# Performance work log

Hardware: AMD Instinct MI355X
Metric: run time of the kernel (lower is better)

## Reference

```python
import jax, jax.numpy as jnp
import numpy as np

# static configuration (matches init_kwargs)
Z, H, W = 8, 96, 192
WZ, WH, WW = 2, 6, 12
DIM, HEADS, DEPTH = 192, 6, 2
HD = DIM // HEADS
NZ, NH, NW = Z // WZ, H // WH, W // WW
N = WZ * WH * WW            # tokens per window = 144
WT = NZ * NH                 # window_types = 64
SHIFT = (WZ // 2, WH // 2, WW // 2)
SCALE = HD ** -0.5


def _pos_index():
    czi = np.arange(WZ); czj = -np.arange(WZ) * WZ
    chi = np.arange(WH); chj = -np.arange(WH) * WH
    cw = np.arange(WW)
    c1 = np.stack(np.meshgrid(czi, chi, cw, indexing='ij'), 0).reshape(3, -1)
    c2 = np.stack(np.meshgrid(czj, chj, cw, indexing='ij'), 0).reshape(3, -1)
    coords = (c1[:, :, None] - c2[:, None, :]).transpose(1, 2, 0).astype(np.int64)
    coords[:, :, 2] += WW - 1
    coords[:, :, 1] *= 2 * WW - 1
    coords[:, :, 0] *= (2 * WW - 1) * WH * WH
    return coords.sum(-1).reshape(-1).astype(np.int32)


def _shift_mask():
    img = np.zeros((Z, H, W))
    zs = (slice(0, -WZ), slice(-WZ, -SHIFT[0]), slice(-SHIFT[0], None))
    hs = (slice(0, -WH), slice(-WH, -SHIFT[1]), slice(-SHIFT[1], None))
    ws = (slice(0, -WW), slice(-WW, -SHIFT[2]), slice(-SHIFT[2], None))
    cnt = 0
    for a in zs:
        for b in hs:
            for c in ws:
                img[a, b, c] = cnt; cnt += 1
    mw = img.reshape(NZ, WZ, NH, WH, NW, WW).transpose(0, 2, 4, 1, 3, 5).reshape(-1, N)
    am = mw[:, None, :] - mw[:, :, None]
    return np.where(am != 0, -100.0, 0.0).astype(np.float32)  # (WT*NW, N, N)

POS_IDX = jnp.asarray(_pos_index())
MASK = jnp.asarray(_shift_mask())


def _partition(x):
    # (B,Z,H,W,C) -> (B*num_windows, N, C), windows ordered (nZ,nH,nW)
    B, C = x.shape[0], x.shape[-1]
    x = x.reshape(B, NZ, WZ, NH, WH, NW, WW, C).transpose(0, 1, 3, 5, 2, 4, 6, 7)
    return x.reshape(-1, N, C)


def _reverse(w, B):
    C = w.shape[-1]
    x = w.reshape(B, NZ, NH, NW, WZ, WH, WW, C).transpose(0, 1, 4, 2, 5, 3, 6, 7)
    return x.reshape(B, Z, H, W, C)


def _ln(x, s, b):
    m = x.mean(-1, keepdims=True)
    v = ((x - m) ** 2).mean(-1, keepdims=True)
    return (x - m) * jax.lax.rsqrt(v + 1e-5) * s + b


def _attention(xw, qw, qb, bias_tab, pw, pb, masked):
    B_ = xw.shape[0]
    qkv = (xw @ qw + qb).reshape(B_, N, 3, HEADS, HD).transpose(2, 0, 3, 1, 4)
    q, k, v = qkv[0] * SCALE, qkv[1], qkv[2]              # (B_, H, N, hd)
    s = jnp.einsum('bhnd,bhmd->bhnm', q, k)               # (B_, H, N, N)
    # earth-specific relative position bias, gathered per window type
    bias = bias_tab[POS_IDX].reshape(N, N, WT, HEADS).transpose(2, 3, 0, 1)  # (WT,H,N,N)
    B = B_ // (WT * NW)
    s = s.reshape(B, WT, NW, HEADS, N, N) + bias[None, :, None]
    if masked:
        s = s + MASK.reshape(WT, NW, N, N)[None, :, :, None]
    a = jax.nn.softmax(s.reshape(B_, HEADS, N, N), axis=-1)
    o = jnp.einsum('bhnm,bhmd->bnhd', a, v).reshape(B_, N, DIM)
    return o @ pw + pb


def _block(x, p, roll):
    n1w, n1b, qw, qb, bt, pw, pb, n2w, n2b, w1, b1, w2, b2 = p
    B = x.shape[0]
    h = _ln(x, n1w, n1b).reshape(B, Z, H, W, DIM)
    if roll:
        h = jnp.roll(h, (-SHIFT[0], -SHIFT[1], -SHIFT[2]), axis=(1, 2, 3))
    h = _attention(_partition(h), qw, qb, bt, pw, pb, roll)
    h = _reverse(h, B)
    if roll:
        h = jnp.roll(h, SHIFT, axis=(1, 2, 3))
    x = x + h.reshape(B, Z * H * W, DIM)
    h2 = _ln(x, n2w, n2b)
    h2 = jax.nn.gelu(h2 @ w1 + b1, approximate=False) @ w2 + b2
    return x + h2


def setup_inputs() -> dict:
    key = jax.random.key(0)
    ks = jax.random.split(key, 8)
    d = {
        'x': jax.random.normal(ks[0], (1, Z * H * W, DIM), jnp.float32),
        'norm1_w': jnp.ones((DEPTH, DIM), jnp.float32),
        'norm1_b': jnp.zeros((DEPTH, DIM), jnp.float32),
        'qkv_w': jax.random.normal(ks[1], (DEPTH, DIM, 3 * DIM), jnp.float32) * 0.02,
        'qkv_b': jnp.zeros((DEPTH, 3 * DIM), jnp.float32),
        'bias_tab': jax.random.normal(ks[2], (DEPTH, WZ**2 * WH**2 * (2 * WW - 1), WT, HEADS), jnp.float32) * 0.02,
        'proj_w': jax.random.normal(ks[3], (DEPTH, DIM, DIM), jnp.float32) * 0.02,
        'proj_b': jnp.zeros((DEPTH, DIM), jnp.float32),
        'norm2_w': jnp.ones((DEPTH, DIM), jnp.float32),
        'norm2_b': jnp.zeros((DEPTH, DIM), jnp.float32),
        'mlp_w1': jax.random.normal(ks[4], (DEPTH, DIM, 4 * DIM), jnp.float32) * 0.02,
        'mlp_b1': jnp.zeros((DEPTH, 4 * DIM), jnp.float32),
        'mlp_w2': jax.random.normal(ks[5], (DEPTH, 4 * DIM, DIM), jnp.float32) * 0.02,
        'mlp_b2': jnp.zeros((DEPTH, DIM), jnp.float32),
    }
    return d


def reference(x, norm1_w, norm1_b, qkv_w, qkv_b, bias_tab, proj_w, proj_b,
              norm2_w, norm2_b, mlp_w1, mlp_b1, mlp_w2, mlp_b2):
    for i in range(DEPTH):
        p = (norm1_w[i], norm1_b[i], qkv_w[i], qkv_b[i], bias_tab[i], proj_w[i],
             proj_b[i], norm2_w[i], norm2_b[i], mlp_w1[i], mlp_b1[i], mlp_w2[i], mlp_b2[i])
        x = _block(x, p, roll=(i % 2 == 1))
    return x
```

## Files before the change

kernel.cpp:

```cpp
#include <hip/hip_runtime.h>
#include <hip/hip_bf16.h>

typedef short short8 __attribute__((ext_vector_type(8)));
typedef short s4b __attribute__((ext_vector_type(4)));
typedef float floatx4 __attribute__((ext_vector_type(4)));
typedef unsigned int u32;

#define DEVFN static __device__ __forceinline__

constexpr int L_TOK = 147456;
constexpr float ATT_SCALE = 0.17677669529663687f;

DEVFN int win_to_spatial(int t, int sz, int sh, int sw) {
  int w_ = t / 144;
  int n  = t - w_ * 144;
  int nz = w_ >> 8, nh = (w_ >> 4) & 15, nw = w_ & 15;
  int iz = n / 72; int rem = n - iz * 72;
  int ih = rem / 12; int iw = rem - ih * 12;
  int z = nz * 2 + iz + sz;  if (z >= 8)   z -= 8;
  int h = nh * 6 + ih + sh;  if (h >= 96)  h -= 96;
  int wc = nw * 12 + iw + sw; if (wc >= 192) wc -= 192;
  return (z * 96 + h) * 192 + wc;
}

DEVFN void gload16(const void* g, void* l) {
  __builtin_amdgcn_global_load_lds(
      (const __attribute__((address_space(1))) u32*)(g),
      (__attribute__((address_space(3))) u32*)(l), 16, 0, 0);
}

DEVFN void bar_vm14() { asm volatile("s_waitcnt vmcnt(14)\n\ts_barrier" ::: "memory"); }
DEVFN void bar_vm12() { asm volatile("s_waitcnt vmcnt(12)\n\ts_barrier" ::: "memory"); }
DEVFN void bar_vm11() { asm volatile("s_waitcnt vmcnt(11)\n\ts_barrier" ::: "memory"); }
DEVFN void bar_vm10() { asm volatile("s_waitcnt vmcnt(10)\n\ts_barrier" ::: "memory"); }
DEVFN void bar_vm8()  { asm volatile("s_waitcnt vmcnt(8)\n\ts_barrier"  ::: "memory"); }
DEVFN void bar_vm7()  { asm volatile("s_waitcnt vmcnt(7)\n\ts_barrier"  ::: "memory"); }
DEVFN void bar_vm6()  { asm volatile("s_waitcnt vmcnt(6)\n\ts_barrier"  ::: "memory"); }
DEVFN void bar_vm0()  { asm volatile("s_waitcnt vmcnt(0)\n\ts_barrier"  ::: "memory"); }
DEVFN void bar_lg()   { asm volatile("s_waitcnt lgkmcnt(0)\n\ts_barrier" ::: "memory"); }

DEVFN float gelu_fast(float x) {
  float e = __expf(-1.702f * x);
  return x * __fdividef(1.0f, 1.0f + e);
}

__global__ __launch_bounds__(256) void convT4_kernel(
    const float* __restrict__ in0, const float* __restrict__ in1,
    const float* __restrict__ in2, const float* __restrict__ in3,
    __hip_bfloat16* __restrict__ o0, __hip_bfloat16* __restrict__ o1,
    __hip_bfloat16* __restrict__ o2, __hip_bfloat16* __restrict__ o3)
{
  int idx = blockIdx.x * 256 + threadIdx.x;
  const float* in; __hip_bfloat16* out; int K, N;
  if (idx < 110592)      { in = in0; out = o0; K = 192; N = 576; }
  else if (idx < 147456) { in = in1; out = o1; K = 192; N = 192; idx -= 110592; }
  else if (idx < 294912) { in = in2; out = o2; K = 192; N = 768; idx -= 147456; }
  else                   { in = in3; out = o3; K = 768; N = 192; idx -= 294912; }
  int n = idx / K, k = idx - n * K;
  out[idx] = __float2bfloat16(in[(long)k * N + n]);
}

__global__ __launch_bounds__(256) void biaspre_kernel(
    const float* __restrict__ tab, __hip_bfloat16* __restrict__ out)
{
  int t = blockIdx.x;
  int e0 = blockIdx.y * 2304;
  for (int e = e0 + threadIdx.x; e < e0 + 2304; e += 256) {
    int m = e / 144, n = e - m * 144;
    int izn = n / 72, rn = n - izn * 72, ihn = rn / 12, iwn = rn - ihn * 12;
    int izm = m / 72, rm = m - izm * 72, ihm = rm / 12, iwm = rm - ihm * 12;
    int idx = (izn + 2 * izm) * 828 + (ihn + 6 * ihm) * 23 + (iwn - iwm + 11);
    out[(long)t * 20736 + e] = __float2bfloat16(tab[(long)idx * 384 + t]);
  }
}

__global__ __launch_bounds__(512) void qkv_kernel(
    const float* __restrict__ x, const float* __restrict__ nw,
    const float* __restrict__ nb,
    const __hip_bfloat16* __restrict__ wqkvT, const float* __restrict__ qbias,
    __hip_bfloat16* __restrict__ oq, __hip_bfloat16* __restrict__ okk,
    __hip_bfloat16* __restrict__ ov, int sz, int sh, int sw)
{
  __shared__ char a_lds[128 * 384];
  __shared__ char w_lds[64 * 384];
  __shared__ float bias_lds[576];

  int tid = threadIdx.x, lane = tid & 63, wv = tid >> 6;
  int lc = lane & 15, lr = lane >> 4, lr4 = lr * 4;
  long row0 = (long)blockIdx.x * 128;
  const char* Wc = (const char*)wqkvT;

#pragma unroll
  for (int i = 0; i < 3; i++) {
    int ii = i * 8 + wv;
    int p = ii * 1024 + lane * 16;
    int row = p / 384, cb = p - row * 384;
    int sc = (cb >> 4) ^ (row & 7);
    gload16(Wc + (long)row * 384 + sc * 16, w_lds + ii * 1024);
  }
  if (tid < 144) *(float4*)(bias_lds + tid * 4) = *(const float4*)(qbias + tid * 4);

#pragma unroll
  for (int rg = 0; rg < 2; rg++) {
    int row = rg * 64 + (tid >> 3), sub = tid & 7;
    int src = win_to_spatial((int)(row0 + row), sz, sh, sw);
    const float* xp = x + (long)src * 192;
    float4 v[6];
#pragma unroll
    for (int p = 0; p < 3; p++) {
      v[2*p]   = *(const float4*)(xp + p * 64 + sub * 8);
      v[2*p+1] = *(const float4*)(xp + p * 64 + sub * 8 + 4);
    }
    float s = 0.f, sq = 0.f;
#pragma unroll
    for (int i = 0; i < 6; i++) {
      s  += v[i].x + v[i].y + v[i].z + v[i].w;
      sq += v[i].x*v[i].x + v[i].y*v[i].y + v[i].z*v[i].z + v[i].w*v[i].w;
    }
    for (int m = 1; m < 8; m <<= 1) { s += __shfl_xor(s, m); sq += __shfl_xor(sq, m); }
    float mean = s * (1.0f/192.0f);
    float var  = sq * (1.0f/192.0f) - mean * mean;
    float rstd = rsqrtf(var + 1e-5f);
#pragma unroll
    for (int p = 0; p < 3; p++) {
      int ch0 = p * 64 + sub * 8;
      float4 wa = *(const float4*)(nw + ch0), wb_ = *(const float4*)(nw + ch0 + 4);
      float4 ba = *(const float4*)(nb + ch0), bb_ = *(const float4*)(nb + ch0 + 4);
      const float* va = (const float*)&v[2*p];
      const float* wa_p = (const float*)&wa; const float* wb_p = (const float*)&wb_;
      const float* ba_p = (const float*)&ba; const float* bb_p = (const float*)&bb_;
      __hip_bfloat16 tmp[8];
#pragma unroll
      for (int j = 0; j < 4; j++) {
        tmp[j]     = __float2bfloat16((va[j]   - mean) * rstd * wa_p[j] + ba_p[j]);
        tmp[j + 4] = __float2bfloat16((va[j+4] - mean) * rstd * wb_p[j] + bb_p[j]);
      }
      int slot = p * 8 + sub;
      int ss = slot ^ (row & 7);
      *(uint4*)(a_lds + row * 384 + ss * 16) = *(uint4*)tmp;
    }
  }
  __syncthreads();

  int m0 = wv * 16;
  short8 afr[6];
#pragma unroll
  for (int kt = 0; kt < 6; kt++) {
    int ra = m0 + lc;
    afr[kt] = *(const short8*)(a_lds + ra * 384 + ((kt * 4 + lr) ^ (ra & 7)) * 16);
  }
  bar_lg();

#pragma unroll
  for (int i = 0; i < 3; i++) {
    int ii = i * 8 + wv;
    int p = ii * 1024 + lane * 16;
    int row = p / 384, cb = p - row * 384;
    int sc = (cb >> 4) ^ (row & 7);
    gload16(Wc + (long)(64 + row) * 384 + sc * 16, a_lds + ii * 1024);
  }

  for (int pn = 0; pn < 9; pn++) {
    char* wcur = (pn & 1) ? a_lds : w_lds;
    if (pn == 1) bar_vm7(); else if (pn == 8) bar_vm8(); else bar_vm11();
    floatx4 acc[4];
#pragma unroll
    for (int cf = 0; cf < 4; cf++) acc[cf] = {0.f, 0.f, 0.f, 0.f};
#pragma unroll
    for (int kt = 0; kt < 6; kt++)
#pragma unroll
      for (int cf = 0; cf < 4; cf++) {
        int rb = cf * 16 + lc;
        short8 wfr = *(const short8*)(wcur + rb * 384 + ((kt * 4 + lr) ^ (rb & 7)) * 16);
        acc[cf] = __builtin_amdgcn_mfma_f32_16x16x32_bf16(wfr, afr[kt], acc[cf], 0, 0, 0);
      }
    bar_lg();
    if (pn < 7) {
#pragma unroll
      for (int i = 0; i < 3; i++) {
        int ii = i * 8 + wv;
        int p = ii * 1024 + lane * 16;
        int row = p / 384, cb = p - row * 384;
        int sc = (cb >> 4) ^ (row & 7);
        gload16(Wc + (long)((pn + 2) * 64 + row) * 384 + sc * 16, wcur + ii * 1024);
      }
    }
    int sec = pn / 3;
    __hip_bfloat16* dst = (sec == 0) ? oq : ((sec == 1) ? okk : ov);
    float scale = (sec == 0) ? ATT_SCALE : 1.0f;
#pragma unroll
    for (int cf = 0; cf < 4; cf++) {
      int colb = pn * 64 + cf * 16 + lr4;
      float4 bb = *(const float4*)(bias_lds + colb);
      int c0 = colb - sec * 192;
      int head = c0 >> 5, ch = c0 & 31;
      long row = row0 + m0 + lc;
      __hip_bfloat16 tmp[4];
      tmp[0] = __float2bfloat16((acc[cf][0] + bb.x) * scale);
      tmp[1] = __float2bfloat16((acc[cf][1] + bb.y) * scale);
      tmp[2] = __float2bfloat16((acc[cf][2] + bb.z) * scale);
      tmp[3] = __float2bfloat16((acc[cf][3] + bb.w) * scale);
      *(s4b*)(dst + ((long)head * L_TOK + row) * 32 + ch) = *(s4b*)tmp;
    }
  }
}

__global__ __launch_bounds__(256) void proj_kernel(
    const __hip_bfloat16* __restrict__ A, const __hip_bfloat16* __restrict__ BT,
    const float* __restrict__ cbias, const float* __restrict__ xin,
    float* __restrict__ xout, int sz, int sh, int sw)
{
  __shared__ __hip_bfloat16 a_lds[128 * 192];
  __shared__ __hip_bfloat16 b_lds[64 * 192];
  int tid = threadIdx.x, lane = tid & 63, wv = tid >> 6;
  int wm = wv >> 1, wn = wv & 1;
  int lc = lane & 15, lr = lane >> 4, lr4 = lr * 4;
  long rowBase = (long)blockIdx.x * 128;
  int colBase = blockIdx.y * 64;
  floatx4 acc[4][2];
#pragma unroll
  for (int i = 0; i < 4; i++)
#pragma unroll
    for (int j = 0; j < 2; j++) acc[i][j] = {0.f, 0.f, 0.f, 0.f};

  const char* Ac = (const char*)A;
  const char* Bc = (const char*)BT;

#pragma unroll
  for (int i = 0; i < 12; i++) {
    int ii = i * 4 + wv;
    int p = ii * 1024 + lane * 16;
    int row = p / 384, cb = p - row * 384;
    int sc = (cb >> 4) ^ (row & 7);
    int ch = sc * 8; int head = ch >> 5;
    const char* g = Ac + (((long)head * L_TOK + rowBase + row) * 32 + (ch & 31)) * 2;
    gload16(g, (char*)a_lds + ii * 1024);
  }
#pragma unroll
  for (int i = 0; i < 6; i++) {
    int ii = i * 4 + wv;
    int p = ii * 1024 + lane * 16;
    int row = p / 384, cb = p - row * 384;
    int sc = (cb >> 4) ^ (row & 7);
    const char* g = Bc + (colBase + row) * (long)192 * 2 + sc * 16;
    gload16(g, (char*)b_lds + ii * 1024);
  }
  __syncthreads();
#pragma unroll
  for (int kt = 0; kt < 6; kt++) {
    short8 bfr[2];
#pragma unroll
    for (int fn = 0; fn < 2; fn++) {
      int rb = wn * 32 + fn * 16 + lc;
      bfr[fn] = *(const short8*)((const char*)b_lds + rb * 384 + ((kt * 4 + lr) ^ (rb & 7)) * 16);
    }
#pragma unroll
    for (int fm = 0; fm < 4; fm++) {
      int ra = wm * 64 + fm * 16 + lc;
      short8 afr = *(const short8*)((const char*)a_lds + ra * 384 + ((kt * 4 + lr) ^ (ra & 7)) * 16);
#pragma unroll
      for (int fn = 0; fn < 2; fn++)
        acc[fm][fn] = __builtin_amdgcn_mfma_f32_16x16x32_bf16(bfr[fn], afr, acc[fm][fn], 0, 0, 0);
    }
  }

#pragma unroll
  for (int fm = 0; fm < 4; fm++) {
    long row = rowBase + wm * 64 + fm * 16 + lc;
    int dsti = win_to_spatial((int)row, sz, sh, sw);
#pragma unroll
    for (int fn = 0; fn < 2; fn++) {
      int colb = colBase + wn * 32 + fn * 16 + lr4;
      float4 cb4 = *(const float4*)(cbias + colb);
      long di = (long)dsti * 192 + colb;
      float4 xv = *(const float4*)(xin + di);
      float4 ov;
      ov.x = acc[fm][fn][0] + cb4.x + xv.x;
      ov.y = acc[fm][fn][1] + cb4.y + xv.y;
      ov.z = acc[fm][fn][2] + cb4.z + xv.z;
      ov.w = acc[fm][fn][3] + cb4.w + xv.w;
      *(float4*)(xout + di) = ov;
    }
  }
}

__global__ __launch_bounds__(256) void mlp1_kernel(
    const float* __restrict__ x, const float* __restrict__ nw,
    const float* __restrict__ nb,
    const __hip_bfloat16* __restrict__ w1T, const float* __restrict__ b1,
    __hip_bfloat16* __restrict__ T)
{
  __shared__ char a_lds[64 * 384];
  __shared__ char w_lds[64 * 384];
  __shared__ float b1_lds[768];

  int tid = threadIdx.x, lane = tid & 63, wv = tid >> 6;
  int lc = lane & 15, lr = lane >> 4, lr4 = lr * 4;
  long row0 = (long)blockIdx.x * 64;
  const char* Wc = (const char*)w1T;

#pragma unroll
  for (int i = 0; i < 6; i++) {
    int ii = i * 4 + wv;
    int p = ii * 1024 + lane * 16;
    int row = p / 384, cb = p - row * 384;
    int sc = (cb >> 4) ^ (row & 7);
    gload16(Wc + (long)row * 384 + sc * 16, w_lds + ii * 1024);
  }
  if (tid < 192) *(float4*)(b1_lds + tid * 4) = *(const float4*)(b1 + tid * 4);

#pragma unroll
  for (int rg = 0; rg < 2; rg++) {
    int row = rg * 32 + (tid >> 3), sub = tid & 7;
    const float* xp = x + (row0 + row) * 192;
    float4 v[6];
#pragma unroll
    for (int p = 0; p < 3; p++) {
      v[2*p]   = *(const float4*)(xp + p * 64 + sub * 8);
      v[2*p+1] = *(const float4*)(xp + p * 64 + sub * 8 + 4);
    }
    float s = 0.f, sq = 0.f;
#pragma unroll
    for (int i = 0; i < 6; i++) {
      s  += v[i].x + v[i].y + v[i].z + v[i].w;
      sq += v[i].x*v[i].x + v[i].y*v[i].y + v[i].z*v[i].z + v[i].w*v[i].w;
    }
    for (int m = 1; m < 8; m <<= 1) { s += __shfl_xor(s, m); sq += __shfl_xor(sq, m); }
    float mean = s * (1.0f/192.0f);
    float var  = sq * (1.0f/192.0f) - mean * mean;
    float rstd = rsqrtf(var + 1e-5f);
#pragma unroll
    for (int p = 0; p < 3; p++) {
      int ch0 = p * 64 + sub * 8;
      float4 wa = *(const float4*)(nw + ch0), wb_ = *(const float4*)(nw + ch0 + 4);
      float4 ba = *(const float4*)(nb + ch0), bb_ = *(const float4*)(nb + ch0 + 4);
      const float* va = (const float*)&v[2*p];
      const float* wa_p = (const float*)&wa; const float* wb_p = (const float*)&wb_;
      const float* ba_p = (const float*)&ba; const float* bb_p = (const float*)&bb_;
      __hip_bfloat16 tmp[8];
#pragma unroll
      for (int j = 0; j < 4; j++) {
        tmp[j]     = __float2bfloat16((va[j]   - mean) * rstd * wa_p[j] + ba_p[j]);
        tmp[j + 4] = __float2bfloat16((va[j+4] - mean) * rstd * wb_p[j] + bb_p[j]);
      }
      int slot = p * 8 + sub;
      int ss = slot ^ (row & 7);
      *(uint4*)(a_lds + row * 384 + ss * 16) = *(uint4*)tmp;
    }
  }
  __syncthreads();

  int m0 = wv * 16;
  short8 afr[6];
#pragma unroll
  for (int kt = 0; kt < 6; kt++) {
    int ra = m0 + lc;
    afr[kt] = *(const short8*)(a_lds + ra * 384 + ((kt * 4 + lr) ^ (ra & 7)) * 16);
  }
  bar_lg();

#pragma unroll
  for (int i = 0; i < 6; i++) {
    int ii = i * 4 + wv;
    int p = ii * 1024 + lane * 16;
    int row = p / 384, cb = p - row * 384;
    int sc = (cb >> 4) ^ (row & 7);
    gload16(Wc + (long)(64 + row) * 384 + sc * 16, a_lds + ii * 1024);
  }

  for (int pn = 0; pn < 12; pn++) {
    char* wcur = (pn & 1) ? a_lds : w_lds;
    if (pn == 0) bar_vm6();
    else if (pn == 1) bar_vm10();
    else if (pn == 11) bar_vm8();
    else bar_vm14();
    floatx4 acc[4];
#pragma unroll
    for (int cf = 0; cf < 4; cf++) acc[cf] = {0.f, 0.f, 0.f, 0.f};
#pragma unroll
    for (int kt = 0; kt < 6; kt++)
#pragma unroll
      for (int cf = 0; cf < 4; cf++) {
        int rb = cf * 16 + lc;
        short8 wfr = *(const short8*)(wcur + rb * 384 + ((kt * 4 + lr) ^ (rb & 7)) * 16);
        acc[cf] = __builtin_amdgcn_mfma_f32_16x16x32_bf16(wfr, afr[kt], acc[cf], 0, 0, 0);
      }
    bar_lg();
    if (pn < 10) {
#pragma unroll
      for (int i = 0; i < 6; i++) {
        int ii = i * 4 + wv;
        int p = ii * 1024 + lane * 16;
        int row = p / 384, cb = p - row * 384;
        int sc = (cb >> 4) ^ (row & 7);
        gload16(Wc + (long)((pn + 2) * 64 + row) * 384 + sc * 16, wcur + ii * 1024);
      }
    }
#pragma unroll
    for (int cf = 0; cf < 4; cf++) {
      int colb = pn * 64 + cf * 16 + lr4;
      float4 bb = *(const float4*)(b1_lds + colb);
      long row = row0 + m0 + lc;
      __hip_bfloat16 tmp[4];
      tmp[0] = __float2bfloat16(gelu_fast(acc[cf][0] + bb.x));
      tmp[1] = __float2bfloat16(gelu_fast(acc[cf][1] + bb.y));
      tmp[2] = __float2bfloat16(gelu_fast(acc[cf][2] + bb.z));
      tmp[3] = __float2bfloat16(gelu_fast(acc[cf][3] + bb.w));
      *(s4b*)(T + row * 768 + colb) = *(s4b*)tmp;
    }
  }
}

__global__ __launch_bounds__(256) void mlp2_kernel(
    const __hip_bfloat16* __restrict__ T, const __hip_bfloat16* __restrict__ w2T,
    const float* __restrict__ b2, const float* __restrict__ x,
    float* __restrict__ out)
{
  __shared__ char a_lds[64 * 384];
  __shared__ char w_lds0[64 * 384];
  __shared__ char w_lds1[64 * 384];

  int tid = threadIdx.x, lane = tid & 63, wv = tid >> 6;
  int lc = lane & 15, lr = lane >> 4, lr4 = lr * 4;
  long row0 = (long)blockIdx.x * 64;
  const char* Ac = (const char*)T;
  const char* Wc = (const char*)w2T;
  int m0 = wv * 16;

  floatx4 acc[3][4];
#pragma unroll
  for (int np = 0; np < 3; np++)
#pragma unroll
    for (int cf = 0; cf < 4; cf++) acc[np][cf] = {0.f, 0.f, 0.f, 0.f};

  int s_ii = lane * 16;
#define STAGE_A(KP)                                                          \
  {                                                                          \
    _Pragma("unroll")                                                        \
    for (int i = 0; i < 6; i++) {                                            \
      int ii = i * 4 + wv;                                                   \
      int p = ii * 1024 + s_ii;                                              \
      int row = p / 384, cb = p - row * 384;                                 \
      int sc = (cb >> 4) ^ (row & 7);                                        \
      gload16(Ac + (row0 + row) * 1536 + (KP) * 384 + sc * 16,               \
              a_lds + ii * 1024);                                            \
    }                                                                        \
  }
#define STAGE_W(KP, NP, BUF)                                                 \
  {                                                                          \
    _Pragma("unroll")                                                        \
    for (int i = 0; i < 6; i++) {                                            \
      int ii = i * 4 + wv;                                                   \
      int p = ii * 1024 + s_ii;                                              \
      int row = p / 384, cb = p - row * 384;                                 \
      int sc = (cb >> 4) ^ (row & 7);                                        \
      gload16(Wc + (long)((NP) * 64 + row) * 1536 + (KP) * 384 + sc * 16,    \
              (BUF) + ii * 1024);                                            \
    }                                                                        \
  }

  STAGE_A(0);
  STAGE_W(0, 0, w_lds0);
  __syncthreads();
  STAGE_W(0, 1, w_lds1);

#pragma unroll
  for (int kp = 0; kp < 4; kp++) {
    if (kp) bar_vm12();
    short8 afr[6];
#pragma unroll
    for (int kt = 0; kt < 6; kt++) {
      int ra = m0 + lc;
      afr[kt] = *(const short8*)(a_lds + ra * 384 + ((kt * 4 + lr) ^ (ra & 7)) * 16);
    }
    bar_lg();
    if (kp < 3) STAGE_A(kp + 1);

#pragma unroll
    for (int np = 0; np < 3; np++) {
      int g = 3 * kp + np;
      const char* wcur = (g & 1) ? w_lds1 : w_lds0;
      if (g == 11) bar_vm0();
      else if (np == 2 || kp == 3) bar_vm6();
      else bar_vm12();
#pragma unroll
      for (int kt = 0; kt < 6; kt++)
#pragma unroll
        for (int cf = 0; cf < 4; cf++) {
          int rb = cf * 16 + lc;
          short8 wfr = *(const short8*)(wcur + rb * 384 + ((kt * 4 + lr) ^ (rb & 7)) * 16);
          acc[np][cf] = __builtin_amdgcn_mfma_f32_16x16x32_bf16(wfr, afr[kt], acc[np][cf], 0, 0, 0);
        }
      bar_lg();
      int gn = g + 2;
      if (gn < 12) {
        char* bnx = (gn & 1) ? w_lds1 : w_lds0;
        int kpn = gn / 3, npn = gn - kpn * 3;
        STAGE_W(kpn, npn, bnx);
      }
    }
  }

#pragma unroll
  for (int np = 0; np < 3; np++)
#pragma unroll
    for (int cf = 0; cf < 4; cf++) {
      int colb = np * 64 + cf * 16 + lr4;
      long row = row0 + m0 + lc;
      float4 bb = *(const float4*)(b2 + colb);
      float4 xv = *(const float4*)(x + row * 192 + colb);
      float4 ov;
      ov.x = acc[np][cf][0] + bb.x + xv.x;
      ov.y = acc[np][cf][1] + bb.y + xv.y;
      ov.z = acc[np][cf][2] + bb.z + xv.z;
      ov.w = acc[np][cf][3] + bb.w + xv.w;
      *(float4*)(out + row * 192 + colb) = ov;
    }
#undef STAGE_A
#undef STAGE_W
}

__global__ __launch_bounds__(576) void attn_kernel(
    const __hip_bfloat16* __restrict__ q, const __hip_bfloat16* __restrict__ k,
    const __hip_bfloat16* __restrict__ v, const __hip_bfloat16* __restrict__ bias_bf,
    __hip_bfloat16* __restrict__ o, int masked)
{
  __shared__ __hip_bfloat16 vT[2][32 * 168];
  __shared__ __hip_bfloat16 pS[9][16 * 40];

  int bid = blockIdx.x;
  int chunk = bid % 384, half = bid / 384;
  int wt = chunk / 6, head = chunk - wt * 6;

  int tid = threadIdx.x, wv = tid >> 6, lane = tid & 63;
  int lr = lane >> 4, lc = lane & 15, lr4 = lr * 4;
  const __hip_bfloat16 zb = __float2bfloat16(0.0f);
  int rt = wv;

  s4b bias_r[9];
  {
    const __hip_bfloat16* bp = bias_bf + (long)chunk * 20736;
#pragma unroll
    for (int c = 0; c < 9; c++)
      bias_r[c] = *(const s4b*)(bp + (c * 16 + lc) * 144 + rt * 16 + lr4);
  }

  int w0 = wt * 16 + half * 8;
  long hb = (long)head * L_TOK * 32;
  {
    long base0 = hb + (long)w0 * 144 * 32;
    int tk = tid >> 2, c = tid & 3;
    uint4 raw = *(const uint4*)(v + base0 + tk * 32 + c * 8);
    __hip_bfloat16 tmp[8]; *(uint4*)tmp = raw;
#pragma unroll
    for (int j = 0; j < 8; j++) vT[0][(c * 8 + j) * 168 + tk] = tmp[j];
  }
  for (int id = tid; id < 1024; id += 576)
    vT[id >> 9][((id >> 4) & 31) * 168 + 144 + (id & 15)] = zb;

  int sign_[4], sigm_[9];
#pragma unroll
  for (int r = 0; r < 4; r++) {
    int p = rt * 16 + lr4 + r;
    int iz = p / 72; int rem = p - iz * 72; int ih = rem / 12; int iw = rem - ih * 12;
    sign_[r] = iz | ((ih >= 3) << 1) | ((iw >= 6) << 2);
  }
#pragma unroll
  for (int c = 0; c < 9; c++) {
    int p = c * 16 + lc;
    int iz = p / 72; int rem = p - iz * 72; int ih = rem / 12; int iw = rem - ih * 12;
    sigm_[c] = iz | ((ih >= 3) << 1) | ((iw >= 6) << 2);
  }
  bar_lg();

  __hip_bfloat16* pw = &pS[wv][0];
  const floatx4 z4 = {0.f, 0.f, 0.f, 0.f};
  int cur = 0;

  for (int wi = 0; wi < 8; wi++) {
    int w_ = w0 + wi;
    long base = hb + (long)w_ * 144 * 32;
    uint4 vreg;
    if (wi < 7)
      vreg = *(const uint4*)(v + base + 144 * 32 + (tid >> 2) * 32 + (tid & 3) * 8);

    int g = 0;
    if (masked) {
      int nz = w_ >> 8, nh = (w_ >> 4) & 15, nw = w_ & 15;
      g = (nz == 3 ? 1 : 0) | (nh == 15 ? 2 : 0) | (nw == 15 ? 4 : 0);
    }

    short8 qf = *(const short8*)(q + base + (rt * 16 + lc) * 32 + lr * 8);
    floatx4 s[9];
    __builtin_amdgcn_s_setprio(1);
#pragma unroll
    for (int c = 0; c < 9; c++) {
      short8 kf = *(const short8*)(k + base + (c * 16 + lc) * 32 + lr * 8);
      s[c] = __builtin_amdgcn_mfma_f32_16x16x32_bf16(qf, kf, z4, 0, 0, 0);
    }
    __builtin_amdgcn_s_setprio(0);

    float rmax[4] = {-1e30f, -1e30f, -1e30f, -1e30f};
#pragma unroll
    for (int c = 0; c < 9; c++) {
      __hip_bfloat16 bb[4];
      *(s4b*)bb = bias_r[c];
#pragma unroll
      for (int r = 0; r < 4; r++) {
        float val = s[c][r] + __bfloat162float(bb[r]);
        if ((sign_[r] ^ sigm_[c]) & g) val -= 100.0f;
        s[c][r] = val;
        rmax[r] = fmaxf(rmax[r], val);
      }
    }
#pragma unroll
    for (int r = 0; r < 4; r++)
      for (int mm = 1; mm < 16; mm <<= 1) rmax[r] = fmaxf(rmax[r], __shfl_xor(rmax[r], mm));
    float rsum[4] = {0.f, 0.f, 0.f, 0.f};
#pragma unroll
    for (int c = 0; c < 9; c++)
#pragma unroll
      for (int r = 0; r < 4; r++) {
        float p = __expf(s[c][r] - rmax[r]);
        s[c][r] = p; rsum[r] += p;
      }
#pragma unroll
    for (int r = 0; r < 4; r++)
      for (int mm = 1; mm < 16; mm <<= 1) rsum[r] += __shfl_xor(rsum[r], mm);

    if (wi < 7) {
      __hip_bfloat16 tmp[8]; *(uint4*)tmp = vreg;
      int tk = tid >> 2, c = tid & 3;
#pragma unroll
      for (int j = 0; j < 8; j++) vT[cur ^ 1][(c * 8 + j) * 168 + tk] = tmp[j];
    }

    floatx4 oacc[2] = {z4, z4};
#pragma unroll
    for (int t = 0; t < 5; t++) {
      if (t < 4) {
#pragma unroll
        for (int h2 = 0; h2 < 2; h2++) {
          int c = 2 * t + h2;
#pragma unroll
          for (int r = 0; r < 4; r++)
            pw[(lr4 + r) * 40 + h2 * 16 + lc] = __float2bfloat16(s[c][r]);
        }
      } else {
#pragma unroll
        for (int r = 0; r < 4; r++) {
          pw[(lr4 + r) * 40 + lc] = __float2bfloat16(s[8][r]);
          pw[(lr4 + r) * 40 + 16 + lc] = zb;
        }
      }
      short8 pa = *(short8*)(&pw[lc * 40 + lr * 8]);
      __builtin_amdgcn_s_setprio(1);
#pragma unroll
      for (int vt = 0; vt < 2; vt++) {
        short8 vbf = *(short8*)(&vT[cur][(vt * 16 + lc) * 168 + t * 32 + lr * 8]);
        oacc[vt] = __builtin_amdgcn_mfma_f32_16x16x32_bf16(pa, vbf, oacc[vt], 0, 0, 0);
      }
      __builtin_amdgcn_s_setprio(0);
    }
    float inv[4];
#pragma unroll
    for (int r = 0; r < 4; r++) inv[r] = 1.0f / rsum[r];
#pragma unroll
    for (int vt = 0; vt < 2; vt++)
#pragma unroll
      for (int r = 0; r < 4; r++)
        o[base + (rt * 16 + lr4 + r) * 32 + vt * 16 + lc] =
            __float2bfloat16(oacc[vt][r] * inv[r]);

    bar_lg();
    cur ^= 1;
  }
}

extern "C" void kernel_launch(void* const* d_in, const int* in_sizes, int n_in,
                              void* d_out, int out_size, void* d_ws, size_t ws_size,
                              hipStream_t stream)
{
  const float* x_in  = (const float*)d_in[0];
  const float* n1w   = (const float*)d_in[1];
  const float* n1b   = (const float*)d_in[2];
  const float* qkvw  = (const float*)d_in[3];
  const float* qkvb  = (const float*)d_in[4];
  const float* btab  = (const float*)d_in[5];
  const float* projw = (const float*)d_in[6];
  const float* projb = (const float*)d_in[7];
  const float* n2w   = (const float*)d_in[8];
  const float* n2b   = (const float*)d_in[9];
  const float* w1    = (const float*)d_in[10];
  const float* b1    = (const float*)d_in[11];
  const float* w2    = (const float*)d_in[12];
  const float* b2    = (const float*)d_in[13];

  char* ws = (char*)d_ws;
  float* x            = (float*)(ws);
  __hip_bfloat16* qb  = (__hip_bfloat16*)(ws + 169869312);
  __hip_bfloat16* kb  = qb + 28311552;
  __hip_bfloat16* vb  = kb + 28311552;
  __hip_bfloat16* ob  = vb + 28311552;
  __hip_bfloat16* Tb  = qb;
  __hip_bfloat16* biasb = (__hip_bfloat16*)(ws + 396361728);
  __hip_bfloat16* wqkvT  = (__hip_bfloat16*)(ws + 428212224);
  __hip_bfloat16* wprojT = wqkvT + 110592;
  __hip_bfloat16* w1T    = wprojT + 36864;
  __hip_bfloat16* w2T    = w1T + 147456;

  for (int layer = 0; layer < 2; layer++) {
    int sz = layer ? 1 : 0, sh = layer ? 3 : 0, sw = layer ? 6 : 0;
    int masked = layer;
    const float* xsrc = (layer == 0) ? x_in : x;

    convT4_kernel<<<1728, 256, 0, stream>>>(
        qkvw + (long)layer * 110592, projw + (long)layer * 36864,
        w1 + (long)layer * 147456, w2 + (long)layer * 147456,
        wqkvT, wprojT, w1T, w2T);
    biaspre_kernel<<<dim3(384, 9), 256, 0, stream>>>(btab + (long)layer * 3312 * 384, biasb);

    qkv_kernel<<<1152, 512, 0, stream>>>(
        xsrc, n1w + layer * 192, n1b + layer * 192, wqkvT, qkvb + layer * 576,
        qb, kb, vb, sz, sh, sw);
    attn_kernel<<<768, 576, 0, stream>>>(qb, kb, vb, biasb, ob, masked);
    proj_kernel<<<dim3(1152, 3), 256, 0, stream>>>(
        ob, wprojT, projb + layer * 192, xsrc, x, sz, sh, sw);
    mlp1_kernel<<<2304, 256, 0, stream>>>(
        x, n2w + layer * 192, n2b + layer * 192, w1T, b1 + layer * 768, Tb);
    mlp2_kernel<<<2304, 256, 0, stream>>>(
        Tb, w2T, b2 + layer * 192, x, (layer == 0) ? x : (float*)d_out);
  }
}
```

Measured before the change: 1.154 ms.

## Process two windows per iteration in attention kernel for more ILP

The attention kernel now handles two windows per loop iteration instead of one, interleaving their QK MFMAs, softmax, and PV MFMAs so independent work can hide latency. V tiles for both windows are staged into the two LDS buffers, replacing the single-window double buffer, and the prefetched V for the next pair is written after a barrier, followed by a second barrier. This halves loop trips and barriers per window but roughly doubles register pressure, which may hurt occupancy. It also loses the previous overlap of V transposition with compute.

```diff
diff --git a/kernel.cpp b/kernel.cpp
--- a/kernel.cpp
+++ b/kernel.cpp
@@ -526,7 +526,7 @@
     __hip_bfloat16* __restrict__ o, int masked)
 {
   __shared__ __hip_bfloat16 vT[2][32 * 168];
-  __shared__ __hip_bfloat16 pS[9][16 * 40];
+  __shared__ __hip_bfloat16 pS[2][9][16 * 40];
 
   int bid = blockIdx.x;
   int chunk = bid % 384, half = bid / 384;
@@ -548,12 +548,15 @@
   int w0 = wt * 16 + half * 8;
   long hb = (long)head * L_TOK * 32;
   {
-    long base0 = hb + (long)w0 * 144 * 32;
     int tk = tid >> 2, c = tid & 3;
-    uint4 raw = *(const uint4*)(v + base0 + tk * 32 + c * 8);
-    __hip_bfloat16 tmp[8]; *(uint4*)tmp = raw;
-#pragma unroll
-    for (int j = 0; j < 8; j++) vT[0][(c * 8 + j) * 168 + tk] = tmp[j];
+#pragma unroll
+    for (int b = 0; b < 2; b++) {
+      long base0 = hb + (long)(w0 + b) * 144 * 32;
+      uint4 raw = *(const uint4*)(v + base0 + tk * 32 + c * 8);
+      __hip_bfloat16 tmp[8]; *(uint4*)tmp = raw;
+#pragma unroll
+      for (int j = 0; j < 8; j++) vT[b][(c * 8 + j) * 168 + tk] = tmp[j];
+    }
   }
   for (int id = tid; id < 1024; id += 576)
     vT[id >> 9][((id >> 4) & 31) * 168 + 144 + (id & 15)] = zb;
@@ -573,69 +576,79 @@
   }
   bar_lg();
 
-  __hip_bfloat16* pw = &pS[wv][0];
+  __hip_bfloat16* pwA = &pS[0][wv][0];
+  __hip_bfloat16* pwB = &pS[1][wv][0];
   const floatx4 z4 = {0.f, 0.f, 0.f, 0.f};
-  int cur = 0;
-
-  for (int wi = 0; wi < 8; wi++) {
-    int w_ = w0 + wi;
-    long base = hb + (long)w_ * 144 * 32;
-    uint4 vreg;
-    if (wi < 7)
-      vreg = *(const uint4*)(v + base + 144 * 32 + (tid >> 2) * 32 + (tid & 3) * 8);
-
-    int g = 0;
+
+  for (int j4 = 0; j4 < 4; j4++) {
+    int wA = w0 + 2 * j4, wB = wA + 1;
+    long baseA = hb + (long)wA * 144 * 32;
+    long baseB = hb + (long)wB * 144 * 32;
+    uint4 vregA, vregB;
+    if (j4 < 3) {
+      vregA = *(const uint4*)(v + baseA + 2 * 144 * 32 + (tid >> 2) * 32 + (tid & 3) * 8);
+      vregB = *(const uint4*)(v + baseB + 2 * 144 * 32 + (tid >> 2) * 32 + (tid & 3) * 8);
+    }
+    int gA = 0, gB = 0;
     if (masked) {
-      int nz = w_ >> 8, nh = (w_ >> 4) & 15, nw = w_ & 15;
-      g = (nz == 3 ? 1 : 0) | (nh == 15 ? 2 : 0) | (nw == 15 ? 4 : 0);
-    }
-
-    short8 qf = *(const short8*)(q + base + (rt * 16 + lc) * 32 + lr * 8);
-    floatx4 s[9];
+      { int nz = wA >> 8, nh = (wA >> 4) & 15, nw = wA & 15;
+        gA = (nz == 3 ? 1 : 0) | (nh == 15 ? 2 : 0) | (nw == 15 ? 4 : 0); }
+      { int nz = wB >> 8, nh = (wB >> 4) & 15, nw = wB & 15;
+        gB = (nz == 3 ? 1 : 0) | (nh == 15 ? 2 : 0) | (nw == 15 ? 4 : 0); }
+    }
+
+    short8 qfA = *(const short8*)(q + baseA + (rt * 16 + lc) * 32 + lr * 8);
+    short8 qfB = *(const short8*)(q + baseB + (rt * 16 + lc) * 32 + lr * 8);
+    floatx4 sA[9], sB[9];
     __builtin_amdgcn_s_setprio(1);
 #pragma unroll
     for (int c = 0; c < 9; c++) {
-      short8 kf = *(const short8*)(k + base + (c * 16 + lc) * 32 + lr * 8);
-      s[c] = __builtin_amdgcn_mfma_f32_16x16x32_bf16(qf, kf, z4, 0, 0, 0);
+      short8 kfA = *(const short8*)(k + baseA + (c * 16 + lc) * 32 + lr * 8);
+      sA[c] = __builtin_amdgcn_mfma_f32_16x16x32_bf16(qfA, kfA, z4, 0, 0, 0);
+      short8 kfB = *(const short8*)(k + baseB + (c * 16 + lc) * 32 + lr * 8);
+      sB[c] = __builtin_amdgcn_mfma_f32_16x16x32_bf16(qfB, kfB, z4, 0, 0, 0);
     }
     __builtin_amdgcn_s_setprio(0);
 
-    float rmax[4] = {-1e30f, -1e30f, -1e30f, -1e30f};
+    float rmaxA[4] = {-1e30f, -1e30f, -1e30f, -1e30f};
+    float rmaxB[4] = {-1e30f, -1e30f, -1e30f, -1e30f};
 #pragma unroll
     for (int c = 0; c < 9; c++) {
       __hip_bfloat16 bb[4];
       *(s4b*)bb = bias_r[c];
 #pragma unroll
       for (int r = 0; r < 4; r++) {
-        float val = s[c][r] + __bfloat162float(bb[r]);
-        if ((sign_[r] ^ sigm_[c]) & g) val -= 100.0f;
-        s[c][r] = val;
-        rmax[r] = fmaxf(rmax[r], val);
+        float bf = __bfloat162float(bb[r]);
+        int msk = (sign_[r] ^ sigm_[c]);
+        float vA = sA[c][r] + bf; if (msk & gA) vA -= 100.0f;
+        float vB = sB[c][r] + bf; if (msk & gB) vB -= 100.0f;
+        sA[c][r] = vA; rmaxA[r] = fmaxf(rmaxA[r], vA);
+        sB[c][r] = vB; rmaxB[r] = fmaxf(rmaxB[r], vB);
       }
     }
 #pragma unroll
     for (int r = 0; r < 4; r++)
-      for (int mm = 1; mm < 16; mm <<= 1) rmax[r] = fmaxf(rmax[r], __shfl_xor(rmax[r], mm));
-    float rsum[4] = {0.f, 0.f, 0.f, 0.f};
+      for (int mm = 1; mm < 16; mm <<= 1) {
+        rmaxA[r] = fmaxf(rmaxA[r], __shfl_xor(rmaxA[r], mm));
+        rmaxB[r] = fmaxf(rmaxB[r], __shfl_xor(rmaxB[r], mm));
+      }
+    float rsumA[4] = {0.f, 0.f, 0.f, 0.f};
+    float rsumB[4] = {0.f, 0.f, 0.f, 0.f};
 #pragma unroll
     for (int c = 0; c < 9; c++)
 #pragma unroll
       for (int r = 0; r < 4; r++) {
-        float p = __expf(s[c][r] - rmax[r]);
-        s[c][r] = p; rsum[r] += p;
+        float pA = __expf(sA[c][r] - rmaxA[r]); sA[c][r] = pA; rsumA[r] += pA;
+        float pB = __expf(sB[c][r] - rmaxB[r]); sB[c][r] = pB; rsumB[r] += pB;
       }
 #pragma unroll
     for (int r = 0; r < 4; r++)
-      for (int mm = 1; mm < 16; mm <<= 1) rsum[r] += __shfl_xor(rsum[r], mm);
-
-    if (wi < 7) {
-      __hip_bfloat16 tmp[8]; *(uint4*)tmp = vreg;
-      int tk = tid >> 2, c = tid & 3;
-#pragma unroll
-      for (int j = 0; j < 8; j++) vT[cur ^ 1][(c * 8 + j) * 168 + tk] = tmp[j];
-    }
-
-    floatx4 oacc[2] = {z4, z4};
+      for (int mm = 1; mm < 16; mm <<= 1) {
+        rsumA[r] += __shfl_xor(rsumA[r], mm);
+        rsumB[r] += __shfl_xor(rsumB[r], mm);
+      }
+
+    floatx4 oaccA[2] = {z4, z4}, oaccB[2] = {z4, z4};
 #pragma unroll
     for (int t = 0; t < 5; t++) {
       if (t < 4) {
@@ -643,37 +656,60 @@
         for (int h2 = 0; h2 < 2; h2++) {
           int c = 2 * t + h2;
 #pragma unroll
-          for (int r = 0; r < 4; r++)
-            pw[(lr4 + r) * 40 + h2 * 16 + lc] = __float2bfloat16(s[c][r]);
+          for (int r = 0; r < 4; r++) {
+            pwA[(lr4 + r) * 40 + h2 * 16 + lc] = __float2bfloat16(sA[c][r]);
+            pwB[(lr4 + r) * 40 + h2 * 16 + lc] = __float2bfloat16(sB[c][r]);
+          }
         }
       } else {
 #pragma unroll
         for (int r = 0; r < 4; r++) {
-          pw[(lr4 + r) * 40 + lc] = __float2bfloat16(s[8][r]);
-          pw[(lr4 + r) * 40 + 16 + lc] = zb;
+          pwA[(lr4 + r) * 40 + lc] = __float2bfloat16(sA[8][r]);
+          pwA[(lr4 + r) * 40 + 16 + lc] = zb;
+          pwB[(lr4 + r) * 40 + lc] = __float2bfloat16(sB[8][r]);
+          pwB[(lr4 + r) * 40 + 16 + lc] = zb;
         }
       }
-      short8 pa = *(short8*)(&pw[lc * 40 + lr * 8]);
+      short8 paA = *(short8*)(&pwA[lc * 40 + lr * 8]);
+      short8 paB = *(short8*)(&pwB[lc * 40 + lr * 8]);
       __builtin_amdgcn_s_setprio(1);
 #pragma unroll
       for (int vt = 0; vt < 2; vt++) {
-        short8 vbf = *(short8*)(&vT[cur][(vt * 16 + lc) * 168 + t * 32 + lr * 8]);
-        oacc[vt] = __builtin_amdgcn_mfma_f32_16x16x32_bf16(pa, vbf, oacc[vt], 0, 0, 0);
+        short8 vbfA = *(short8*)(&vT[0][(vt * 16 + lc) * 168 + t * 32 + lr * 8]);
+        oaccA[vt] = __builtin_amdgcn_mfma_f32_16x16x32_bf16(paA, vbfA, oaccA[vt], 0, 0, 0);
+        short8 vbfB = *(short8*)(&vT[1][(vt * 16 + lc) * 168 + t * 32 + lr * 8]);
+        oaccB[vt] = __builtin_amdgcn_mfma_f32_16x16x32_bf16(paB, vbfB, oaccB[vt], 0, 0, 0);
       }
       __builtin_amdgcn_s_setprio(0);
     }
-    float inv[4];
-#pragma unroll
-    for (int r = 0; r < 4; r++) inv[r] = 1.0f / rsum[r];
+    float invA[4], invB[4];
+#pragma unroll
+    for (int r = 0; r < 4; r++) {
+      invA[r] = 1.0f / rsumA[r];
+      invB[r] = 1.0f / rsumB[r];
+    }
 #pragma unroll
     for (int vt = 0; vt < 2; vt++)
 #pragma unroll
-      for (int r = 0; r < 4; r++)
-        o[base + (rt * 16 + lr4 + r) * 32 + vt * 16 + lc] =
-            __float2bfloat16(oacc[vt][r] * inv[r]);
+      for (int r = 0; r < 4; r++) {
+        o[baseA + (rt * 16 + lr4 + r) * 32 + vt * 16 + lc] =
+            __float2bfloat16(oaccA[vt][r] * invA[r]);
+        o[baseB + (rt * 16 + lr4 + r) * 32 + vt * 16 + lc] =
+            __float2bfloat16(oaccB[vt][r] * invB[r]);
+      }
 
     bar_lg();
-    cur ^= 1;
+    if (j4 < 3) {
+      int tk = tid >> 2, c = tid & 3;
+      __hip_bfloat16 tA[8]; *(uint4*)tA = vregA;
+      __hip_bfloat16 tB[8]; *(uint4*)tB = vregB;
+#pragma unroll
+      for (int j = 0; j < 8; j++) {
+        vT[0][(c * 8 + j) * 168 + tk] = tA[j];
+        vT[1][(c * 8 + j) * 168 + tk] = tB[j];
+      }
+      bar_lg();
+    }
   }
 }
 
```

Result: slower. 1.396 ms (+21.0%).
